# Performance work log

Measured on AMD Instinct MI355X. Metric: run time of the kernel, lower is better.

## Reference

```python
import jax, jax.numpy as jnp
import numpy as np

N = 100_000      # nodes
E = 3_200_000    # edges (avg degree 32)
F_IN = 37        # NCI1 num_features
H = 16           # hidden
C = 2            # NCI1 num_classes


def setup_inputs() -> dict:
    key = jax.random.key(0)
    k = jax.random.split(key, 7)
    x = jax.random.normal(k[0], (N, F_IN), dtype=jnp.float32)
    edge_index = jax.random.randint(k[1], (2, E), 0, N, dtype=jnp.int32)
    edge_weight = jax.random.uniform(k[2], (E,), dtype=jnp.float32)
    # Glorot-ish init for the two GCN linear weights, zero bias (PyG default)
    W1 = jax.random.normal(k[3], (F_IN, H), dtype=jnp.float32) * (1.0 / np.sqrt(F_IN))
    b1 = jnp.zeros((H,), dtype=jnp.float32)
    W2 = jax.random.normal(k[4], (H, C), dtype=jnp.float32) * (1.0 / np.sqrt(H))
    b2 = jnp.zeros((C,), dtype=jnp.float32)
    return {"x": x, "edge_index": edge_index, "edge_weight": edge_weight,
            "W1": W1, "b1": b1, "W2": W2, "b2": b2}


def _gcn_norm(edge_index, edge_weight, dtype):
    # PyG gcn_norm: add self-loops (weight 1.0), symmetric D^-1/2 A D^-1/2
    loop = jnp.arange(N, dtype=edge_index.dtype)
    row = jnp.concatenate([edge_index[0], loop])  # source
    col = jnp.concatenate([edge_index[1], loop])  # target (aggregation index)
    w = jnp.concatenate([edge_weight, jnp.ones((N,), dtype=dtype)])
    deg = jax.ops.segment_sum(w, col, num_segments=N)
    dinv = jnp.where(deg > 0, jax.lax.rsqrt(deg), 0.0).astype(dtype)
    norm = dinv[row] * w * dinv[col]  # [E+N]
    return row, col, norm


def _gcn_layer(x, row, col, norm, W, b):
    h = x @ W                                   # small dense transform first
    msg = norm[:, None] * h[row]                # gather + scale, [E+N, out]
    out = jax.ops.segment_sum(msg, col, num_segments=N)  # scatter-add
    return out + b


def reference(x, edge_index, edge_weight, W1, b1, W2, b2):
    row, col, norm = _gcn_norm(edge_index, edge_weight, x.dtype)
    h = jax.nn.relu(_gcn_layer(x, row, col, norm, W1, b1))
    # F.dropout with training=False is identity (module evaluated in eval mode)
    h = _gcn_layer(h, row, col, norm, W2, b2)
    return jax.nn.log_softmax(h, axis=1)
```

## Files before the change

### kernel.cpp

```cpp
#include <hip/hip_runtime.h>
#include <math.h>

#define N_NODES 100000
#define N_EDGES 3200000
#define F_IN    37
#define H_DIM   16
#define C_DIM   2

#define BUCKET_BITS 7
#define BUCKET_SZ   128
#define NBUCK       782
#define CAP         4736
#define NPBLK       512
#define EB          6250
#define EPT_P       7
#define EPT_S       5

__device__ __forceinline__ unsigned bf16rne(float f) {
    unsigned u = __float_as_uint(f);
    return (u + 0x7FFFu + ((u >> 16) & 1u)) >> 16;
}
__device__ __forceinline__ int2 ldnt_i2(const int2* p) {
    long long v = __builtin_nontemporal_load((const long long*)p);
    return *(int2*)&v;
}
#define BLO(u) __uint_as_float((u) << 16)
#define BHI(u) __uint_as_float((u) & 0xFFFF0000u)
#define EW(u)  __uint_as_float(((u) >> 17) << 16)
#define ER(u)  ((u) & 0x1FFFFu)

__global__ __launch_bounds__(1024) void k_part(
    const int* __restrict__ row, const int* __restrict__ col,
    const float* __restrict__ w, int* __restrict__ gcur, int2* __restrict__ ebuf)
{
    __shared__ int  cnt[NBUCK];
    __shared__ int  base[NBUCK];
    __shared__ int  gbase[NBUCK];
    __shared__ int2 stage[EB];
    int t = threadIdx.x;
    size_t e0 = (size_t)blockIdx.x * EB;
    int bk[EPT_P], rc[EPT_P], lofs[EPT_P];
    float wv[EPT_P];

    if (t < NBUCK) cnt[t] = 0;
    __syncthreads();
#pragma unroll
    for (int k = 0; k < EPT_P; k++) {
        int i = k * 1024 + t;
        if (i < EB) {
            size_t e = e0 + i;
            int r = __builtin_nontemporal_load(&row[e]);
            int c = __builtin_nontemporal_load(&col[e]);
            wv[k] = __builtin_nontemporal_load(&w[e]);
            bk[k] = c >> BUCKET_BITS;
            rc[k] = r | ((c & (BUCKET_SZ - 1)) << 17);
            lofs[k] = atomicAdd(&cnt[bk[k]], 1);
        } else bk[k] = -1;
    }
    __syncthreads();
    if (t < NBUCK) base[t] = cnt[t];
    __syncthreads();
    for (int off = 1; off < 1024; off <<= 1) {
        int v = 0;
        if (t < NBUCK && t >= off) v = base[t - off];
        __syncthreads();
        if (t < NBUCK) base[t] += v;
        __syncthreads();
    }
#pragma unroll
    for (int k = 0; k < EPT_P; k++) {
        if (bk[k] >= 0)
            stage[base[bk[k]] - cnt[bk[k]] + lofs[k]] =
                make_int2(rc[k], __float_as_int(wv[k]));
    }
    if (t < NBUCK) gbase[t] = t * CAP + atomicAdd(&gcur[t], cnt[t]);
    __syncthreads();
    for (int s2 = t; s2 < EB; s2 += 1024) {
        int lo = 0, hi = NBUCK - 1;
        while (lo < hi) { int mid = (lo + hi) >> 1; if (base[mid] > s2) hi = mid; else lo = mid + 1; }
        int dst = gbase[lo] + (s2 - (base[lo] - cnt[lo]));
        ebuf[dst] = stage[s2];
    }
}

__global__ __launch_bounds__(1024) void k_sortxw1(
    const int* __restrict__ gcur, const int2* __restrict__ ebuf,
    const float* __restrict__ x, const float* __restrict__ W1,
    unsigned* __restrict__ ebuf4, int2* __restrict__ rp,
    float* __restrict__ dinv, unsigned* __restrict__ h1b)
{
    __shared__ int2  stage[CAP];
    __shared__ int   cnt[BUCKET_SZ];
    __shared__ int   base[BUCKET_SZ];
    __shared__ float sdinv[BUCKET_SZ];
    __shared__ float sW[F_IN * H_DIM];
    float* xs = (float*)stage;

    int t = threadIdx.x, b = blockIdx.x;
    int s = b * CAP;
    int len = gcur[b];
    int nbase = b << BUCKET_BITS;
    if (t < BUCKET_SZ) cnt[t] = 0;
    __syncthreads();

    int2 ed[EPT_S]; int cl[EPT_S], lofs[EPT_S];
#pragma unroll
    for (int k = 0; k < EPT_S; k++) {
        int i = k * 1024 + t;
        if (i < len) {
            int2 v = ldnt_i2(&ebuf[s + i]);
            ed[k] = v;
            cl[k] = v.x >> 17;
            lofs[k] = atomicAdd(&cnt[cl[k]], 1);
        } else cl[k] = -1;
    }
    __syncthreads();
    if (t < BUCKET_SZ) base[t] = cnt[t];
    __syncthreads();
    for (int off = 1; off < BUCKET_SZ; off <<= 1) {
        int v2 = 0;
        if (t < BUCKET_SZ && t >= off) v2 = base[t - off];
        __syncthreads();
        if (t < BUCKET_SZ) base[t] += v2;
        __syncthreads();
    }
#pragma unroll
    for (int k = 0; k < EPT_S; k++) {
        if (cl[k] >= 0) {
            int pos = base[cl[k]] - cnt[cl[k]] + lofs[k];
            stage[pos] = ed[k];
        }
    }
    __syncthreads();
    for (int i = t; i < len; i += 1024) {
        int2 v = stage[i];
        unsigned wb = bf16rne(__int_as_float(v.y));
        __builtin_nontemporal_store((wb << 17) | (unsigned)(v.x & 0x1FFFF),
                                    &ebuf4[s + i]);
    }
    {
        int n = t >> 3, l = t & 7;
        int st = base[n] - cnt[n], cn = cnt[n];
        float sum = 0.f;
        for (int i = l; i < cn; i += 8) sum += __int_as_float(stage[st + i].y);
        sum += __shfl_xor(sum, 1);
        sum += __shfl_xor(sum, 2);
        sum += __shfl_xor(sum, 4);
        if (l == 0) {
            float di = rsqrtf(sum + 1.0f);
            sdinv[n] = di;
            int c = nbase + n;
            if (c < N_NODES) {
                rp[c] = make_int2(s + st, cn);
                dinv[c] = di;
            }
        }
    }
    __syncthreads();

    for (int idx = t; idx < F_IN * H_DIM; idx += 1024) sW[idx] = W1[idx];
    {
        const float4* x4 = (const float4*)(x + (size_t)nbase * F_IN);
        const int nv4 = (BUCKET_SZ * F_IN) / 4;
        int gf0 = nbase * F_IN;
        for (int idx = t; idx < nv4; idx += 1024) {
            int gf = gf0 + 4 * idx;
            float4 v;
            if (gf + 3 < N_NODES * F_IN) {
                v = x4[idx];
            } else {
                v.x = (gf + 0 < N_NODES * F_IN) ? x[gf + 0] : 0.f;
                v.y = (gf + 1 < N_NODES * F_IN) ? x[gf + 1] : 0.f;
                v.z = (gf + 2 < N_NODES * F_IN) ? x[gf + 2] : 0.f;
                v.w = (gf + 3 < N_NODES * F_IN) ? x[gf + 3] : 0.f;
            }
            ((float4*)xs)[idx] = v;
        }
    }
    __syncthreads();
    {
        int n = t >> 3, sub = t & 7;
        int c = nbase + n;
        if (c < N_NODES) {
            const float* xi = &xs[n * F_IN];
            float a0 = 0.f, a1 = 0.f;
            for (int k = 0; k < F_IN; k++) {
                float xv = xi[k];
                a0 += xv * sW[k * H_DIM + 2 * sub];
                a1 += xv * sW[k * H_DIM + 2 * sub + 1];
            }
            float di = sdinv[n];
            unsigned pk = bf16rne(di * a0) | (bf16rne(di * a1) << 16);
            h1b[(size_t)c * 8 + sub] = pk;
        }
    }
}

__global__ __launch_bounds__(256) void k_agg1(
    const int2* __restrict__ rp, const unsigned* __restrict__ ebuf4,
    const uint4* __restrict__ h1b, const float* __restrict__ dinv,
    const float* __restrict__ b1, const float* __restrict__ W2,
    float* __restrict__ h2s)
{
    __shared__ float sW2[H_DIM * C_DIM];
    __shared__ float sb1[H_DIM];
    int t = threadIdx.x;
    if (t < H_DIM * C_DIM) sW2[t] = W2[t];
    if (t >= 32 && t < 32 + H_DIM) sb1[t - 32] = b1[t - 32];
    __syncthreads();
    int id = blockIdx.x * 256 + t;
    int c = id >> 4;
    int sub = id & 15, q = sub & 1, h = sub >> 1;
    if (c >= N_NODES) return;
    int2 seg = rp[c];
    int s = seg.x, n = seg.y;
    int m = (n - h + 7) >> 3;
    int p0i = s + h;
    float acc[8] = {0.f, 0.f, 0.f, 0.f, 0.f, 0.f, 0.f, 0.f};

#define PROC1(u)                                                    \
    {   float a = EW(u);                                            \
        uint4 g = h1b[(size_t)ER(u) * 2 + q];                       \
        acc[0] += a * BLO(g.x); acc[1] += a * BHI(g.x);             \
        acc[2] += a * BLO(g.y); acc[3] += a * BHI(g.y);             \
        acc[4] += a * BLO(g.z); acc[5] += a * BHI(g.z);             \
        acc[6] += a * BLO(g.w); acc[7] += a * BHI(g.w); }

    int k = 0;
    if (m >= 4) {
        unsigned e0 = __builtin_nontemporal_load(&ebuf4[p0i + 0]);
        unsigned e1 = __builtin_nontemporal_load(&ebuf4[p0i + 8]);
        unsigned e2 = __builtin_nontemporal_load(&ebuf4[p0i + 16]);
        unsigned e3 = __builtin_nontemporal_load(&ebuf4[p0i + 24]);
        for (; k + 8 <= m; k += 4) {
            unsigned f0 = __builtin_nontemporal_load(&ebuf4[p0i + 8 * (k + 4)]);
            unsigned f1 = __builtin_nontemporal_load(&ebuf4[p0i + 8 * (k + 5)]);
            unsigned f2 = __builtin_nontemporal_load(&ebuf4[p0i + 8 * (k + 6)]);
            unsigned f3 = __builtin_nontemporal_load(&ebuf4[p0i + 8 * (k + 7)]);
            PROC1(e0); PROC1(e1); PROC1(e2); PROC1(e3);
            e0 = f0; e1 = f1; e2 = f2; e3 = f3;
        }
        PROC1(e0); PROC1(e1); PROC1(e2); PROC1(e3);
        k += 4;
    }
    for (; k < m; k++) {
        unsigned u = __builtin_nontemporal_load(&ebuf4[p0i + 8 * k]);
        PROC1(u);
    }
#undef PROC1

#pragma unroll
    for (int j = 0; j < 8; j++) {
        acc[j] += __shfl_xor(acc[j], 2);
        acc[j] += __shfl_xor(acc[j], 4);
        acc[j] += __shfl_xor(acc[j], 8);
    }

    float dc = dinv[c];
    uint4 gc = h1b[(size_t)c * 2 + q];
    float hcv[8] = {BLO(gc.x), BHI(gc.x), BLO(gc.y), BHI(gc.y),
                    BLO(gc.z), BHI(gc.z), BLO(gc.w), BHI(gc.w)};
    int j0 = q << 3;
    float p0 = 0.f, p1 = 0.f;
#pragma unroll
    for (int j = 0; j < 8; j++) {
        float rv = fmaxf(dc * (acc[j] + hcv[j]) + sb1[j0 + j], 0.f);
        p0 += rv * sW2[(j0 + j) * C_DIM + 0];
        p1 += rv * sW2[(j0 + j) * C_DIM + 1];
    }
    p0 += __shfl_xor(p0, 1);
    p1 += __shfl_xor(p1, 1);
    if (sub == 0) ((float2*)h2s)[c] = make_float2(dc * p0, dc * p1);
}

__global__ __launch_bounds__(256) void k_agg2(
    const int2* __restrict__ rp, const unsigned* __restrict__ ebuf4,
    const float* __restrict__ h2s, const float* __restrict__ dinv,
    const float* __restrict__ b2, float* __restrict__ out)
{
    int id = blockIdx.x * 256 + threadIdx.x;
    int c = id >> 3, sub = id & 7;
    if (c >= N_NODES) return;
    int2 seg = rp[c];
    int s = seg.x, n = seg.y;
    const float2* h22 = (const float2*)h2s;
    int m = (n - sub + 7) >> 3;
    int p0i = s + sub;
    float a0 = 0.f, a1 = 0.f;

#define PROC2(u)                                                    \
    {   float a = EW(u);                                            \
        float2 hv = h22[ER(u)];                                     \
        a0 += a * hv.x;  a1 += a * hv.y; }

    int k = 0;
    if (m >= 4) {
        unsigned e0 = __builtin_nontemporal_load(&ebuf4[p0i + 0]);
        unsigned e1 = __builtin_nontemporal_load(&ebuf4[p0i + 8]);
        unsigned e2 = __builtin_nontemporal_load(&ebuf4[p0i + 16]);
        unsigned e3 = __builtin_nontemporal_load(&ebuf4[p0i + 24]);
        for (; k + 8 <= m; k += 4) {
            unsigned f0 = __builtin_nontemporal_load(&ebuf4[p0i + 8 * (k + 4)]);
            unsigned f1 = __builtin_nontemporal_load(&ebuf4[p0i + 8 * (k + 5)]);
            unsigned f2 = __builtin_nontemporal_load(&ebuf4[p0i + 8 * (k + 6)]);
            unsigned f3 = __builtin_nontemporal_load(&ebuf4[p0i + 8 * (k + 7)]);
            PROC2(e0); PROC2(e1); PROC2(e2); PROC2(e3);
            e0 = f0; e1 = f1; e2 = f2; e3 = f3;
        }
        PROC2(e0); PROC2(e1); PROC2(e2); PROC2(e3);
        k += 4;
    }
    for (; k < m; k++) {
        unsigned u = __builtin_nontemporal_load(&ebuf4[p0i + 8 * k]);
        PROC2(u);
    }
#undef PROC2

    a0 += __shfl_xor(a0, 1); a0 += __shfl_xor(a0, 2); a0 += __shfl_xor(a0, 4);
    a1 += __shfl_xor(a1, 1); a1 += __shfl_xor(a1, 2); a1 += __shfl_xor(a1, 4);
    if (sub == 0) {
        float dc = dinv[c];
        float2 hc = h22[c];
        float l0 = dc * (a0 + hc.x) + b2[0];
        float l1 = dc * (a1 + hc.y) + b2[1];
        float mx = fmaxf(l0, l1);
        float lse = mx + logf(expf(l0 - mx) + expf(l1 - mx));
        ((float2*)out)[c] = make_float2(l0 - lse, l1 - lse);
    }
}

extern "C" void kernel_launch(void* const* d_in, const int* in_sizes, int n_in,
                              void* d_out, int out_size, void* d_ws, size_t ws_size,
                              hipStream_t stream) {
    const float* x  = (const float*)d_in[0];
    const int*   ei = (const int*)d_in[1];
    const float* w  = (const float*)d_in[2];
    const float* W1 = (const float*)d_in[3];
    const float* b1 = (const float*)d_in[4];
    const float* W2 = (const float*)d_in[5];
    const float* b2 = (const float*)d_in[6];
    float* out = (float*)d_out;

    const int* row = ei;
    const int* col = ei + N_EDGES;

    char* ws = (char*)d_ws;
    int*      gcur  = (int*)(ws + 0);
    int2*     rp    = (int2*)(ws + 3200);
    float*    dinv  = (float*)(ws + 803200);
    unsigned* h1b   = (unsigned*)(ws + 1203200);
    float*    h2s   = (float*)(ws + 4403200);
    unsigned* ebuf4 = (unsigned*)(ws + 5203200);
    int2*     ebuf  = (int2*)(ws + 20017408);

    hipMemsetAsync(gcur, 0, 3200, stream);
    k_part    <<<NPBLK, 1024, 0, stream>>>(row, col, w, gcur, ebuf);
    k_sortxw1 <<<NBUCK, 1024, 0, stream>>>(gcur, ebuf, x, W1, ebuf4, rp, dinv, h1b);
    k_agg1    <<<(16 * N_NODES + 255) / 256, 256, 0, stream>>>(rp, ebuf4, (const uint4*)h1b, dinv, b1, W2, h2s);
    k_agg2    <<<(8 * N_NODES + 255) / 256, 256, 0, stream>>>(rp, ebuf4, h2s, dinv, b2, out);
}
```

Before: 193.9 us.

## Replace two-pass bucket sort with histogram, scan, and atomic scatter CSR build

Swaps the partition-then-local-sort CSR construction for a global histogram that packs the edge count and a fixed-point weight sum into one 64-bit atomic per destination node. A two-level prefix scan then yields per-node offsets, and a scatter kernel places each edge with a per-node atomic cursor. This removes the intermediate int2 edge buffer and the shared-memory sorting passes, but adds global atomics and makes edge order within a row nondeterministic. The fixed-point weight sum also changes rounding of the degree slightly.

```diff
diff --git a/kernel.cpp b/kernel.cpp
--- a/kernel.cpp
+++ b/kernel.cpp
@@ -9,155 +9,111 @@
 
 #define BUCKET_BITS 7
 #define BUCKET_SZ   128
-#define NBUCK       782
-#define CAP         4736
-#define NPBLK       512
-#define EB          6250
-#define EPT_P       7
-#define EPT_S       5
+#define NXW1        782
+#define NSCAN       98
+
+#define CNT_SHIFT 42
+#define WSUM_MASK ((1ull << CNT_SHIFT) - 1)
 
 __device__ __forceinline__ unsigned bf16rne(float f) {
     unsigned u = __float_as_uint(f);
     return (u + 0x7FFFu + ((u >> 16) & 1u)) >> 16;
-}
-__device__ __forceinline__ int2 ldnt_i2(const int2* p) {
-    long long v = __builtin_nontemporal_load((const long long*)p);
-    return *(int2*)&v;
 }
 #define BLO(u) __uint_as_float((u) << 16)
 #define BHI(u) __uint_as_float((u) & 0xFFFF0000u)
 #define EW(u)  __uint_as_float(((u) >> 17) << 16)
 #define ER(u)  ((u) & 0x1FFFFu)
 
-__global__ __launch_bounds__(1024) void k_part(
-    const int* __restrict__ row, const int* __restrict__ col,
-    const float* __restrict__ w, int* __restrict__ gcur, int2* __restrict__ ebuf)
-{
-    __shared__ int  cnt[NBUCK];
-    __shared__ int  base[NBUCK];
-    __shared__ int  gbase[NBUCK];
-    __shared__ int2 stage[EB];
+__global__ __launch_bounds__(256) void k_hist(
+    const int* __restrict__ col, const float* __restrict__ w,
+    unsigned long long* __restrict__ acc)
+{
+    int i = blockIdx.x * 256 + threadIdx.x;
+    const int4   c4 = ((const int4*)col)[i];
+    const float4 w4 = ((const float4*)w)[i];
+    atomicAdd(&acc[c4.x], (1ull << CNT_SHIFT) | (unsigned long long)(w4.x * 4294967296.0f));
+    atomicAdd(&acc[c4.y], (1ull << CNT_SHIFT) | (unsigned long long)(w4.y * 4294967296.0f));
+    atomicAdd(&acc[c4.z], (1ull << CNT_SHIFT) | (unsigned long long)(w4.z * 4294967296.0f));
+    atomicAdd(&acc[c4.w], (1ull << CNT_SHIFT) | (unsigned long long)(w4.w * 4294967296.0f));
+}
+
+__global__ __launch_bounds__(1024) void k_scan1(
+    const unsigned long long* __restrict__ acc,
+    int* __restrict__ tmpbase, int* __restrict__ partial)
+{
+    __shared__ int wscan[16];
+    int t = threadIdx.x, n = blockIdx.x * 1024 + t;
+    int c = (n < N_NODES) ? (int)(acc[n] >> CNT_SHIFT) : 0;
+    int lane = t & 63, wid = t >> 6;
+    int v = c;
+#pragma unroll
+    for (int d = 1; d < 64; d <<= 1) {
+        int u = __shfl_up(v, d);
+        if (lane >= d) v += u;
+    }
+    if (lane == 63) wscan[wid] = v;
+    __syncthreads();
+    if (wid == 0) {
+        int u = (lane < 16) ? wscan[lane] : 0;
+#pragma unroll
+        for (int d = 1; d < 16; d <<= 1) {
+            int u2 = __shfl_up(u, d);
+            if (lane >= d) u += u2;
+        }
+        if (lane < 16) wscan[lane] = u;
+    }
+    __syncthreads();
+    int incl = v + ((wid > 0) ? wscan[wid - 1] : 0);
+    tmpbase[n] = incl - c;
+    if (t == 1023) partial[blockIdx.x] = incl;
+}
+
+__global__ __launch_bounds__(128) void k_scan2(
+    const int* __restrict__ partial, int* __restrict__ blockoff)
+{
+    __shared__ int ws2[2];
     int t = threadIdx.x;
-    size_t e0 = (size_t)blockIdx.x * EB;
-    int bk[EPT_P], rc[EPT_P], lofs[EPT_P];
-    float wv[EPT_P];
-
-    if (t < NBUCK) cnt[t] = 0;
-    __syncthreads();
-#pragma unroll
-    for (int k = 0; k < EPT_P; k++) {
-        int i = k * 1024 + t;
-        if (i < EB) {
-            size_t e = e0 + i;
-            int r = __builtin_nontemporal_load(&row[e]);
-            int c = __builtin_nontemporal_load(&col[e]);
-            wv[k] = __builtin_nontemporal_load(&w[e]);
-            bk[k] = c >> BUCKET_BITS;
-            rc[k] = r | ((c & (BUCKET_SZ - 1)) << 17);
-            lofs[k] = atomicAdd(&cnt[bk[k]], 1);
-        } else bk[k] = -1;
-    }
-    __syncthreads();
-    if (t < NBUCK) base[t] = cnt[t];
-    __syncthreads();
-    for (int off = 1; off < 1024; off <<= 1) {
-        int v = 0;
-        if (t < NBUCK && t >= off) v = base[t - off];
-        __syncthreads();
-        if (t < NBUCK) base[t] += v;
-        __syncthreads();
-    }
-#pragma unroll
-    for (int k = 0; k < EPT_P; k++) {
-        if (bk[k] >= 0)
-            stage[base[bk[k]] - cnt[bk[k]] + lofs[k]] =
-                make_int2(rc[k], __float_as_int(wv[k]));
-    }
-    if (t < NBUCK) gbase[t] = t * CAP + atomicAdd(&gcur[t], cnt[t]);
-    __syncthreads();
-    for (int s2 = t; s2 < EB; s2 += 1024) {
-        int lo = 0, hi = NBUCK - 1;
-        while (lo < hi) { int mid = (lo + hi) >> 1; if (base[mid] > s2) hi = mid; else lo = mid + 1; }
-        int dst = gbase[lo] + (s2 - (base[lo] - cnt[lo]));
-        ebuf[dst] = stage[s2];
-    }
-}
-
-__global__ __launch_bounds__(1024) void k_sortxw1(
-    const int* __restrict__ gcur, const int2* __restrict__ ebuf,
+    int c = (t < NSCAN) ? partial[t] : 0;
+    int lane = t & 63, wid = t >> 6;
+    int v = c;
+#pragma unroll
+    for (int d = 1; d < 64; d <<= 1) {
+        int u = __shfl_up(v, d);
+        if (lane >= d) v += u;
+    }
+    if (lane == 63) ws2[wid] = v;
+    __syncthreads();
+    int incl = v + ((wid > 0) ? ws2[0] : 0);
+    if (t < NSCAN) blockoff[t] = incl - c;
+}
+
+__global__ __launch_bounds__(1024) void k_xw1(
+    const unsigned long long* __restrict__ acc,
+    const int* __restrict__ tmpbase, const int* __restrict__ blockoff,
     const float* __restrict__ x, const float* __restrict__ W1,
-    unsigned* __restrict__ ebuf4, int2* __restrict__ rp,
+    int2* __restrict__ rp, int* __restrict__ cur,
     float* __restrict__ dinv, unsigned* __restrict__ h1b)
 {
-    __shared__ int2  stage[CAP];
-    __shared__ int   cnt[BUCKET_SZ];
-    __shared__ int   base[BUCKET_SZ];
+    __shared__ float xs[BUCKET_SZ * F_IN];
+    __shared__ float sW[F_IN * H_DIM];
     __shared__ float sdinv[BUCKET_SZ];
-    __shared__ float sW[F_IN * H_DIM];
-    float* xs = (float*)stage;
-
     int t = threadIdx.x, b = blockIdx.x;
-    int s = b * CAP;
-    int len = gcur[b];
     int nbase = b << BUCKET_BITS;
-    if (t < BUCKET_SZ) cnt[t] = 0;
-    __syncthreads();
-
-    int2 ed[EPT_S]; int cl[EPT_S], lofs[EPT_S];
-#pragma unroll
-    for (int k = 0; k < EPT_S; k++) {
-        int i = k * 1024 + t;
-        if (i < len) {
-            int2 v = ldnt_i2(&ebuf[s + i]);
-            ed[k] = v;
-            cl[k] = v.x >> 17;
-            lofs[k] = atomicAdd(&cnt[cl[k]], 1);
-        } else cl[k] = -1;
-    }
-    __syncthreads();
-    if (t < BUCKET_SZ) base[t] = cnt[t];
-    __syncthreads();
-    for (int off = 1; off < BUCKET_SZ; off <<= 1) {
-        int v2 = 0;
-        if (t < BUCKET_SZ && t >= off) v2 = base[t - off];
-        __syncthreads();
-        if (t < BUCKET_SZ) base[t] += v2;
-        __syncthreads();
-    }
-#pragma unroll
-    for (int k = 0; k < EPT_S; k++) {
-        if (cl[k] >= 0) {
-            int pos = base[cl[k]] - cnt[cl[k]] + lofs[k];
-            stage[pos] = ed[k];
-        }
-    }
-    __syncthreads();
-    for (int i = t; i < len; i += 1024) {
-        int2 v = stage[i];
-        unsigned wb = bf16rne(__int_as_float(v.y));
-        __builtin_nontemporal_store((wb << 17) | (unsigned)(v.x & 0x1FFFF),
-                                    &ebuf4[s + i]);
-    }
-    {
-        int n = t >> 3, l = t & 7;
-        int st = base[n] - cnt[n], cn = cnt[n];
-        float sum = 0.f;
-        for (int i = l; i < cn; i += 8) sum += __int_as_float(stage[st + i].y);
-        sum += __shfl_xor(sum, 1);
-        sum += __shfl_xor(sum, 2);
-        sum += __shfl_xor(sum, 4);
-        if (l == 0) {
-            float di = rsqrtf(sum + 1.0f);
-            sdinv[n] = di;
-            int c = nbase + n;
-            if (c < N_NODES) {
-                rp[c] = make_int2(s + st, cn);
-                dinv[c] = di;
-            }
-        }
-    }
-    __syncthreads();
-
+
+    if (t < BUCKET_SZ) {
+        int c = nbase + t;
+        if (c < N_NODES) {
+            unsigned long long a = acc[c];
+            int cn = (int)(a >> CNT_SHIFT);
+            float wsum = (float)(a & WSUM_MASK) * 2.3283064365386963e-10f;
+            float di = rsqrtf(wsum + 1.0f);
+            sdinv[t] = di;
+            int base = tmpbase[c] + blockoff[c >> 10];
+            rp[c] = make_int2(base, cn);
+            cur[c] = base;
+            dinv[c] = di;
+        }
+    }
     for (int idx = t; idx < F_IN * H_DIM; idx += 1024) sW[idx] = W1[idx];
     {
         const float4* x4 = (const float4*)(x + (size_t)nbase * F_IN);
@@ -196,6 +152,19 @@
     }
 }
 
+__global__ __launch_bounds__(256) void k_scatter(
+    const int* __restrict__ row, const int* __restrict__ col,
+    const float* __restrict__ w, int* __restrict__ cur,
+    unsigned* __restrict__ ebuf4)
+{
+    int e = blockIdx.x * 256 + threadIdx.x;
+    int r = __builtin_nontemporal_load(&row[e]);
+    int c = __builtin_nontemporal_load(&col[e]);
+    float wv = __builtin_nontemporal_load(&w[e]);
+    int pos = atomicAdd(&cur[c], 1);
+    ebuf4[pos] = (bf16rne(wv) << 17) | (unsigned)r;
+}
+
 __global__ __launch_bounds__(256) void k_agg1(
     const int2* __restrict__ rp, const unsigned* __restrict__ ebuf4,
     const uint4* __restrict__ h1b, const float* __restrict__ dinv,
@@ -345,17 +314,23 @@
     const int* col = ei + N_EDGES;
 
     char* ws = (char*)d_ws;
-    int*      gcur  = (int*)(ws + 0);
-    int2*     rp    = (int2*)(ws + 3200);
-    float*    dinv  = (float*)(ws + 803200);
-    unsigned* h1b   = (unsigned*)(ws + 1203200);
-    float*    h2s   = (float*)(ws + 4403200);
-    unsigned* ebuf4 = (unsigned*)(ws + 5203200);
-    int2*     ebuf  = (int2*)(ws + 20017408);
-
-    hipMemsetAsync(gcur, 0, 3200, stream);
-    k_part    <<<NPBLK, 1024, 0, stream>>>(row, col, w, gcur, ebuf);
-    k_sortxw1 <<<NBUCK, 1024, 0, stream>>>(gcur, ebuf, x, W1, ebuf4, rp, dinv, h1b);
+    unsigned long long* acc = (unsigned long long*)(ws + 0);
+    int*      tmpbase = (int*)(ws + 802816);
+    int*      blockoff= (int*)(ws + 1204224);
+    int*      partial = (int*)(ws + 1204736);
+    int*      cur     = (int*)(ws + 1205248);
+    int2*     rp      = (int2*)(ws + 1605248);
+    float*    dinv    = (float*)(ws + 2405248);
+    unsigned* h1b     = (unsigned*)(ws + 2805248);
+    float*    h2s     = (float*)(ws + 6005248);
+    unsigned* ebuf4   = (unsigned*)(ws + 6805248);
+
+    hipMemsetAsync(acc, 0, 802816, stream);
+    k_hist    <<<3125, 256, 0, stream>>>(col, w, acc);
+    k_scan1   <<<NSCAN, 1024, 0, stream>>>(acc, tmpbase, partial);
+    k_scan2   <<<1, 128, 0, stream>>>(partial, blockoff);
+    k_xw1     <<<NXW1, 1024, 0, stream>>>(acc, tmpbase, blockoff, x, W1, rp, cur, dinv, h1b);
+    k_scatter <<<12500, 256, 0, stream>>>(row, col, w, cur, ebuf4);
     k_agg1    <<<(16 * N_NODES + 255) / 256, 256, 0, stream>>>(rp, ebuf4, (const uint4*)h1b, dinv, b1, W2, h2s);
     k_agg2    <<<(8 * N_NODES + 255) / 256, 256, 0, stream>>>(rp, ebuf4, h2s, dinv, b2, out);
 }
```

New measurement: 547.9 us. 183% more time.
